# Optimization experiments

Measured on AMD Instinct MI355X. Metric: run time of the kernel, lower is better.

The kernel has to match this reference:

```python
import jax, jax.numpy as jnp
import numpy as np

B, N_Q, N_K, DIM = 4, 4096, 4096, 256
INNER = 64
N_TOPK = 3
MINUS_INF = -1e9


def setup_inputs() -> dict:
    key = jax.random.key(0)
    ks = jax.random.split(key, 5)
    q = jax.random.normal(ks[0], (B, N_Q, DIM), dtype=jnp.float32)
    k = jax.random.normal(ks[1], (B, N_K, DIM), dtype=jnp.float32)
    v = jax.random.normal(ks[2], (B, N_K, DIM), dtype=jnp.float32)
    Wq = jax.random.normal(ks[3], (DIM, INNER), dtype=jnp.float32) * 0.02
    Wk = jax.random.normal(ks[4], (DIM, INNER), dtype=jnp.float32) * 0.02
    return {"q": q, "k": k, "v": v, "Wq": Wq, "Wk": Wk}


def reference(q, k, v, Wq, Wk):
    # v is accepted but unused, matching the torch module.
    scale = INNER ** (-0.5)  # dim_head == inner_dim == 64
    qh = (q @ Wq) * scale            # [B, N_Q, 64]
    kh = k @ Wk                      # [B, N_K, 64]
    # heads = 1 -> scores [B, 1, N_Q, N_K]
    scores = jnp.einsum('bqd,bkd->bqk', qh, kh)[:, None]
    # torch.kthvalue(k=N_K - 3) == 4th-largest value per row
    thresh = jax.lax.top_k(scores, N_TOPK + 1)[0][..., N_TOPK:N_TOPK + 1]
    masked = jnp.where(scores < thresh, MINUS_INF, scores)
    return jax.nn.softmax(masked, axis=-1)
```

## Files before the change

### kernel.cpp

```cpp
#include <hip/hip_runtime.h>
#include <hip/hip_bf16.h>
#include <math.h>

typedef float v4f __attribute__((ext_vector_type(4)));
typedef short bf16x8 __attribute__((ext_vector_type(8)));
typedef float f32x16 __attribute__((ext_vector_type(16)));

#define BATCH 4
#define NQ 4096
#define NK 4096
#define DIM 256
#define INNER 64
#define NEG_INF (-3.0e38f)
#define CAP 64

__global__ __launch_bounds__(256) void proj_kernel(
    const float* __restrict__ q, const float* __restrict__ k,
    const float* __restrict__ Wq, const float* __restrict__ Wk,
    float* __restrict__ qh, float* __restrict__ kh,
    ushort* __restrict__ qhb, ushort* __restrict__ khb,
    float* __restrict__ outz)
{
  __shared__ float xs[32 * 260];
  const int bid = blockIdx.x;
  const bool isq = bid < 512;
  const float* X   = isq ? q : k;
  const float* W   = isq ? Wq : Wk;
  float*   out     = isq ? qh : kh;
  const float scale = isq ? 0.125f : 1.0f;
  const int row0 = (isq ? bid : bid - 512) * 32;
  const int t = threadIdx.x;

  #pragma unroll
  for (int it = 0; it < 8; ++it) {
    int idx = it * 256 + t;
    int r = idx >> 6, dq = idx & 63;
    v4f v = *reinterpret_cast<const v4f*>(X + (size_t)(row0 + r) * DIM + dq * 4);
    *reinterpret_cast<v4f*>(&xs[r * 260 + dq * 4]) = v;
  }
  __syncthreads();

  const int i0 = (t & 15) * 4;
  const int rg = t >> 4;
  float acc[2][4];
  #pragma unroll
  for (int p = 0; p < 2; ++p)
    #pragma unroll
    for (int i = 0; i < 4; ++i) acc[p][i] = 0.f;

  for (int d0 = 0; d0 < DIM; d0 += 4) {
    v4f w0 = *reinterpret_cast<const v4f*>(W + (d0 + 0) * INNER + i0);
    v4f w1 = *reinterpret_cast<const v4f*>(W + (d0 + 1) * INNER + i0);
    v4f w2 = *reinterpret_cast<const v4f*>(W + (d0 + 2) * INNER + i0);
    v4f w3 = *reinterpret_cast<const v4f*>(W + (d0 + 3) * INNER + i0);
    #pragma unroll
    for (int p = 0; p < 2; ++p) {
      v4f x = *reinterpret_cast<const v4f*>(&xs[(rg + 16 * p) * 260 + d0]);
      #pragma unroll
      for (int i = 0; i < 4; ++i) {
        float bs = x[0] * w0[i];
        bs = fmaf(x[1], w1[i], bs);
        bs = fmaf(x[2], w2[i], bs);
        bs = fmaf(x[3], w3[i], bs);
        acc[p][i] += bs;
      }
    }
  }

  const int d  = i0 >> 4;
  const int hi = (i0 >> 3) & 1;
  const int e0 = i0 & 7;
  #pragma unroll
  for (int p = 0; p < 2; ++p) {
    v4f o;
    ushort ob[4];
    #pragma unroll
    for (int i = 0; i < 4; ++i) {
      o[i] = acc[p][i] * scale;
      __hip_bfloat16 h = __float2bfloat16(o[i]);
      ob[i] = *reinterpret_cast<ushort*>(&h);
    }
    int rr = rg + 16 * p;
    size_t row = (size_t)(row0 + rr);
    *reinterpret_cast<v4f*>(out + row * INNER + i0) = o;
    if (isq) {
      *reinterpret_cast<uint2*>(qhb + row * INNER + i0) =
          *reinterpret_cast<uint2*>(ob);
    } else {
      size_t off = (size_t)(bid - 512) * 2048 + d * 512 + hi * 256 + rr * 8 + e0;
      *reinterpret_cast<uint2*>(khb + off) = *reinterpret_cast<uint2*>(ob);
    }
  }

  {
    v4f* zp = reinterpret_cast<v4f*>(outz);
    const v4f z = {0.f, 0.f, 0.f, 0.f};
    size_t idx = (size_t)bid * 256 + t;
    #pragma unroll 4
    for (int it = 0; it < 64; ++it)
      zp[idx + (size_t)it * 262144] = z;
  }
}

__device__ __forceinline__ void insert5(float (&v)[5], int (&ix)[5], float x, int xi) {
  bool g0 = x > v[0], g1 = x > v[1], g2 = x > v[2], g3 = x > v[3];
  v[4]  = g3 ? v[3] : x;                 ix[4] = g3 ? ix[3] : xi;
  v[3]  = g3 ? (g2 ? v[2] : x) : v[3];   ix[3] = g3 ? (g2 ? ix[2] : xi) : ix[3];
  v[2]  = g2 ? (g1 ? v[1] : x) : v[2];   ix[2] = g2 ? (g1 ? ix[1] : xi) : ix[2];
  v[1]  = g1 ? (g0 ? v[0] : x) : v[1];   ix[1] = g1 ? (g0 ? ix[0] : xi) : ix[1];
  v[0]  = g0 ? x : v[0];                 ix[0] = g0 ? xi : ix[0];
}

__device__ __forceinline__ void insert8v(float (&v)[8], float x) {
  bool g0 = x > v[0], g1 = x > v[1], g2 = x > v[2], g3 = x > v[3];
  bool g4 = x > v[4], g5 = x > v[5], g6 = x > v[6];
  v[7] = g6 ? v[6] : x;
  v[6] = g6 ? (g5 ? v[5] : x) : v[6];
  v[5] = g5 ? (g4 ? v[4] : x) : v[5];
  v[4] = g4 ? (g3 ? v[3] : x) : v[4];
  v[3] = g3 ? (g2 ? v[2] : x) : v[3];
  v[2] = g2 ? (g1 ? v[1] : x) : v[2];
  v[1] = g1 ? (g0 ? v[0] : x) : v[1];
  v[0] = g0 ? x : v[0];
}

__global__ __launch_bounds__(512) void filter_kernel(
    const ushort* __restrict__ qhb, const ushort* __restrict__ khb,
    const float* __restrict__ qh, const float* __restrict__ kh,
    float* __restrict__ out)
{
  __shared__ float qhf[32][68];
  __shared__ float sm[32][16];
  __shared__ float tau[32];
  __shared__ int   cnt[32];
  __shared__ int   cand[32][CAP];
  __shared__ float exactv[32][CAP];
  __shared__ float w5[32][5];
  __shared__ int   id5[32][6];

  const int t   = threadIdx.x;
  const int bid = blockIdx.x;
  const int wg  = (bid & 7) * 64 + (bid >> 3);
  const int b   = wg >> 7;
  const int q0  = (wg & 127) * 32;
  const int qg  = t >> 6;
  const int kg  = t & 63;
  const int ln  = kg & 31;
  const int hi  = kg >> 5;

  if (t < 256) {
    int row = t >> 3, c8 = (t & 7) * 8;
    const float* src = qh + ((size_t)b * NQ + q0 + row) * INNER + c8;
    *reinterpret_cast<v4f*>(&qhf[row][c8])     = *reinterpret_cast<const v4f*>(src);
    *reinterpret_cast<v4f*>(&qhf[row][c8 + 4]) = *reinterpret_cast<const v4f*>(src + 4);
  }
  if (t < 32) cnt[t] = 0;

  const ushort* qptr = qhb + ((size_t)b * NQ + q0 + ln) * INNER + hi * 8;
  bf16x8 qf0 = *reinterpret_cast<const bf16x8*>(qptr);
  bf16x8 qf1 = *reinterpret_cast<const bf16x8*>(qptr + 16);
  bf16x8 qf2 = *reinterpret_cast<const bf16x8*>(qptr + 32);
  bf16x8 qf3 = *reinterpret_cast<const bf16x8*>(qptr + 48);

  const ushort* ktile = khb + ((size_t)b * 128 + qg * 16) * 2048;

  float smax = NEG_INF;
  for (int t16 = 0; t16 < 16; ++t16) {
    const ushort* tb = ktile + (size_t)t16 * 2048;
    bf16x8 k0 = *reinterpret_cast<const bf16x8*>(tb +        kg * 8);
    bf16x8 k1 = *reinterpret_cast<const bf16x8*>(tb +  512 + kg * 8);
    bf16x8 k2 = *reinterpret_cast<const bf16x8*>(tb + 1024 + kg * 8);
    bf16x8 k3 = *reinterpret_cast<const bf16x8*>(tb + 1536 + kg * 8);

    f32x16 acc = {0.f, 0.f, 0.f, 0.f, 0.f, 0.f, 0.f, 0.f,
                  0.f, 0.f, 0.f, 0.f, 0.f, 0.f, 0.f, 0.f};
    acc = __builtin_amdgcn_mfma_f32_32x32x16_bf16(k0, qf0, acc, 0, 0, 0);
    acc = __builtin_amdgcn_mfma_f32_32x32x16_bf16(k1, qf1, acc, 0, 0, 0);
    acc = __builtin_amdgcn_mfma_f32_32x32x16_bf16(k2, qf2, acc, 0, 0, 0);
    acc = __builtin_amdgcn_mfma_f32_32x32x16_bf16(k3, qf3, acc, 0, 0, 0);

    float m0 = fmaxf(fmaxf(acc[0],  acc[1]),  fmaxf(acc[2],  acc[3]));
    float m1 = fmaxf(fmaxf(acc[4],  acc[5]),  fmaxf(acc[6],  acc[7]));
    float m2 = fmaxf(fmaxf(acc[8],  acc[9]),  fmaxf(acc[10], acc[11]));
    float m3 = fmaxf(fmaxf(acc[12], acc[13]), fmaxf(acc[14], acc[15]));
    smax = fmaxf(smax, fmaxf(fmaxf(m0, m1), fmaxf(m2, m3)));
  }
  sm[ln][qg * 2 + hi] = smax;
  __syncthreads();

  if (t < 32) {
    float rv[8];
    #pragma unroll
    for (int j = 0; j < 8; ++j) rv[j] = NEG_INF;
    #pragma unroll
    for (int s = 0; s < 16; ++s) {
      float x = sm[t][s];
      if (x > rv[7]) insert8v(rv, x);
    }
    tau[t] = rv[7];
  }
  __syncthreads();

  const float tl = tau[ln];
  for (int t16 = 0; t16 < 16; ++t16) {
    const ushort* tb = ktile + (size_t)t16 * 2048;
    bf16x8 k0 = *reinterpret_cast<const bf16x8*>(tb +        kg * 8);
    bf16x8 k1 = *reinterpret_cast<const bf16x8*>(tb +  512 + kg * 8);
    bf16x8 k2 = *reinterpret_cast<const bf16x8*>(tb + 1024 + kg * 8);
    bf16x8 k3 = *reinterpret_cast<const bf16x8*>(tb + 1536 + kg * 8);

    f32x16 acc = {0.f, 0.f, 0.f, 0.f, 0.f, 0.f, 0.f, 0.f,
                  0.f, 0.f, 0.f, 0.f, 0.f, 0.f, 0.f, 0.f};
    acc = __builtin_amdgcn_mfma_f32_32x32x16_bf16(k0, qf0, acc, 0, 0, 0);
    acc = __builtin_amdgcn_mfma_f32_32x32x16_bf16(k1, qf1, acc, 0, 0, 0);
    acc = __builtin_amdgcn_mfma_f32_32x32x16_bf16(k2, qf2, acc, 0, 0, 0);
    acc = __builtin_amdgcn_mfma_f32_32x32x16_bf16(k3, qf3, acc, 0, 0, 0);

    const int kb0 = qg * 512 + t16 * 32 + 4 * hi;
#define CHK(r) { float x_ = acc[r]; \
                 if (x_ >= tl) { \
                   int p_ = atomicAdd(&cnt[ln], 1); \
                   if (p_ < CAP) cand[ln][p_] = kb0 + ((r) & 3) + 8 * ((r) >> 2); } }
    CHK(0)  CHK(1)  CHK(2)  CHK(3)
    CHK(4)  CHK(5)  CHK(6)  CHK(7)
    CHK(8)  CHK(9)  CHK(10) CHK(11)
    CHK(12) CHK(13) CHK(14) CHK(15)
#undef CHK
  }
  __syncthreads();

  {
    int row = t >> 4, j0 = t & 15;
    int n = min(cnt[row], CAP);
    for (int jj = j0; jj < n; jj += 16) {
      int idx = cand[row][jj];
      const float* kcol = kh + ((size_t)b * NK + idx) * INNER;
      float acc = 0.f;
      #pragma unroll
      for (int dd = 0; dd < INNER; dd += 4) {
        v4f kv = *reinterpret_cast<const v4f*>(kcol + dd);
        v4f qv = *reinterpret_cast<const v4f*>(&qhf[row][dd]);
        float bs = qv[0] * kv[0];
        bs = fmaf(qv[1], kv[1], bs);
        bs = fmaf(qv[2], kv[2], bs);
        bs = fmaf(qv[3], kv[3], bs);
        acc += bs;
      }
      exactv[row][jj] = acc;
    }
  }
  __syncthreads();

  if (t < 32) {
    int n = min(cnt[t], CAP);
    float rv[5]; int ri[5];
    #pragma unroll
    for (int j = 0; j < 5; ++j) { rv[j] = NEG_INF; ri[j] = 0; }
    for (int j = 0; j < n; ++j) {
      float x = exactv[t][j];
      if (x > rv[4]) insert5(rv, ri, x, cand[t][j]);
    }
    bool inc4 = (rv[4] >= rv[3]);
    float e1 = expf(rv[1] - rv[0]);
    float e2 = expf(rv[2] - rv[0]);
    float e3 = expf(rv[3] - rv[0]);
    float e4 = inc4 ? expf(rv[4] - rv[0]) : 0.0f;
    float inv = 1.0f / (1.0f + e1 + e2 + e3 + e4);
    w5[t][0] = inv;      w5[t][1] = e1 * inv;  w5[t][2] = e2 * inv;
    w5[t][3] = e3 * inv; w5[t][4] = e4 * inv;
    #pragma unroll
    for (int j = 0; j < 5; ++j) id5[t][j] = ri[j];
    id5[t][5] = inc4 ? 5 : 4;
  }
  __syncthreads();

  if (t < 160) {
    int row = t / 5, j = t % 5;
    if (j < id5[row][5]) {
      float* obase = out + ((size_t)b * NQ + q0) * (size_t)NK;
      obase[(size_t)row * NK + id5[row][j]] = w5[row][j];
    }
  }
}

extern "C" void kernel_launch(void* const* d_in, const int* in_sizes, int n_in,
                              void* d_out, int out_size, void* d_ws, size_t ws_size,
                              hipStream_t stream) {
  const float* q  = (const float*)d_in[0];
  const float* k  = (const float*)d_in[1];
  const float* Wq = (const float*)d_in[3];
  const float* Wk = (const float*)d_in[4];

  const size_t NE = (size_t)BATCH * NQ * INNER;
  float*  qh  = (float*)d_ws;
  float*  kh  = qh + NE;
  ushort* qhb = (ushort*)(kh + NE);
  ushort* khb = qhb + NE;

  proj_kernel<<<1024, 256, 0, stream>>>(q, k, Wq, Wk, qh, kh, qhb, khb,
                                        (float*)d_out);
  filter_kernel<<<512, 512, 0, stream>>>(qhb, khb, qh, kh, (float*)d_out);
}
```

Baseline: 143.1 us.

## Process 64 query rows per filter block and split zero-fill into separate blocks

The filter kernel now handles 64 query rows per workgroup, two 32-row MFMA tiles sharing each loaded K fragment. This halves K-tile reloads and the grid size. The zero-fill of the output moves from the projection blocks into 2048 dedicated blocks, so the fill runs in parallel with projection instead of after it. The cost is more registers and shared memory per filter block and only 256 filter workgroups, which may underfill the GPU.

```diff
diff --git a/kernel.cpp b/kernel.cpp
--- a/kernel.cpp
+++ b/kernel.cpp
@@ -14,7 +14,7 @@
 #define NEG_INF (-3.0e38f)
 #define CAP 64
 
-__global__ __launch_bounds__(256) void proj_kernel(
+__global__ __launch_bounds__(256) void projfill_kernel(
     const float* __restrict__ q, const float* __restrict__ k,
     const float* __restrict__ Wq, const float* __restrict__ Wk,
     float* __restrict__ qh, float* __restrict__ kh,
@@ -23,13 +23,24 @@
 {
   __shared__ float xs[32 * 260];
   const int bid = blockIdx.x;
+  const int t = threadIdx.x;
+
+  if (bid >= 1024) {
+    v4f* zp = reinterpret_cast<v4f*>(outz);
+    const v4f z = {0.f, 0.f, 0.f, 0.f};
+    size_t idx = (size_t)(bid - 1024) * 256 + t;
+    #pragma unroll 8
+    for (int it = 0; it < 32; ++it)
+      zp[idx + (size_t)it * 524288] = z;
+    return;
+  }
+
   const bool isq = bid < 512;
   const float* X   = isq ? q : k;
   const float* W   = isq ? Wq : Wk;
   float*   out     = isq ? qh : kh;
   const float scale = isq ? 0.125f : 1.0f;
   const int row0 = (isq ? bid : bid - 512) * 32;
-  const int t = threadIdx.x;
 
   #pragma unroll
   for (int it = 0; it < 8; ++it) {
@@ -90,15 +101,6 @@
       size_t off = (size_t)(bid - 512) * 2048 + d * 512 + hi * 256 + rr * 8 + e0;
       *reinterpret_cast<uint2*>(khb + off) = *reinterpret_cast<uint2*>(ob);
     }
-  }
-
-  {
-    v4f* zp = reinterpret_cast<v4f*>(outz);
-    const v4f z = {0.f, 0.f, 0.f, 0.f};
-    size_t idx = (size_t)bid * 256 + t;
-    #pragma unroll 4
-    for (int it = 0; it < 64; ++it)
-      zp[idx + (size_t)it * 262144] = z;
   }
 }
 
@@ -129,42 +131,47 @@
     const float* __restrict__ qh, const float* __restrict__ kh,
     float* __restrict__ out)
 {
-  __shared__ float qhf[32][68];
-  __shared__ float sm[32][16];
-  __shared__ float tau[32];
-  __shared__ int   cnt[32];
-  __shared__ int   cand[32][CAP];
-  __shared__ float exactv[32][CAP];
-  __shared__ float w5[32][5];
-  __shared__ int   id5[32][6];
+  __shared__ float qhf[64][68];
+  __shared__ float sm[64][16];
+  __shared__ float tau[64];
+  __shared__ int   cnt[64];
+  __shared__ int   cand[64][CAP];
+  __shared__ float exactv[64][CAP];
+  __shared__ float w5[64][5];
+  __shared__ int   id5[64][6];
 
   const int t   = threadIdx.x;
   const int bid = blockIdx.x;
-  const int wg  = (bid & 7) * 64 + (bid >> 3);
-  const int b   = wg >> 7;
-  const int q0  = (wg & 127) * 32;
+  const int wg  = (bid & 7) * 32 + (bid >> 3);
+  const int b   = wg >> 6;
+  const int q0  = (wg & 63) * 64;
   const int qg  = t >> 6;
   const int kg  = t & 63;
   const int ln  = kg & 31;
   const int hi  = kg >> 5;
 
-  if (t < 256) {
+  {
     int row = t >> 3, c8 = (t & 7) * 8;
     const float* src = qh + ((size_t)b * NQ + q0 + row) * INNER + c8;
     *reinterpret_cast<v4f*>(&qhf[row][c8])     = *reinterpret_cast<const v4f*>(src);
     *reinterpret_cast<v4f*>(&qhf[row][c8 + 4]) = *reinterpret_cast<const v4f*>(src + 4);
   }
-  if (t < 32) cnt[t] = 0;
-
-  const ushort* qptr = qhb + ((size_t)b * NQ + q0 + ln) * INNER + hi * 8;
-  bf16x8 qf0 = *reinterpret_cast<const bf16x8*>(qptr);
-  bf16x8 qf1 = *reinterpret_cast<const bf16x8*>(qptr + 16);
-  bf16x8 qf2 = *reinterpret_cast<const bf16x8*>(qptr + 32);
-  bf16x8 qf3 = *reinterpret_cast<const bf16x8*>(qptr + 48);
+  if (t < 64) cnt[t] = 0;
+
+  const ushort* qptrA = qhb + ((size_t)b * NQ + q0 + ln) * INNER + hi * 8;
+  const ushort* qptrB = qptrA + 32 * INNER;
+  bf16x8 qfA0 = *reinterpret_cast<const bf16x8*>(qptrA);
+  bf16x8 qfA1 = *reinterpret_cast<const bf16x8*>(qptrA + 16);
+  bf16x8 qfA2 = *reinterpret_cast<const bf16x8*>(qptrA + 32);
+  bf16x8 qfA3 = *reinterpret_cast<const bf16x8*>(qptrA + 48);
+  bf16x8 qfB0 = *reinterpret_cast<const bf16x8*>(qptrB);
+  bf16x8 qfB1 = *reinterpret_cast<const bf16x8*>(qptrB + 16);
+  bf16x8 qfB2 = *reinterpret_cast<const bf16x8*>(qptrB + 32);
+  bf16x8 qfB3 = *reinterpret_cast<const bf16x8*>(qptrB + 48);
 
   const ushort* ktile = khb + ((size_t)b * 128 + qg * 16) * 2048;
 
-  float smax = NEG_INF;
+  float smaxA = NEG_INF, smaxB = NEG_INF;
   for (int t16 = 0; t16 < 16; ++t16) {
     const ushort* tb = ktile + (size_t)t16 * 2048;
     bf16x8 k0 = *reinterpret_cast<const bf16x8*>(tb +        kg * 8);
@@ -172,23 +179,33 @@
     bf16x8 k2 = *reinterpret_cast<const bf16x8*>(tb + 1024 + kg * 8);
     bf16x8 k3 = *reinterpret_cast<const bf16x8*>(tb + 1536 + kg * 8);
 
-    f32x16 acc = {0.f, 0.f, 0.f, 0.f, 0.f, 0.f, 0.f, 0.f,
-                  0.f, 0.f, 0.f, 0.f, 0.f, 0.f, 0.f, 0.f};
-    acc = __builtin_amdgcn_mfma_f32_32x32x16_bf16(k0, qf0, acc, 0, 0, 0);
-    acc = __builtin_amdgcn_mfma_f32_32x32x16_bf16(k1, qf1, acc, 0, 0, 0);
-    acc = __builtin_amdgcn_mfma_f32_32x32x16_bf16(k2, qf2, acc, 0, 0, 0);
-    acc = __builtin_amdgcn_mfma_f32_32x32x16_bf16(k3, qf3, acc, 0, 0, 0);
-
-    float m0 = fmaxf(fmaxf(acc[0],  acc[1]),  fmaxf(acc[2],  acc[3]));
-    float m1 = fmaxf(fmaxf(acc[4],  acc[5]),  fmaxf(acc[6],  acc[7]));
-    float m2 = fmaxf(fmaxf(acc[8],  acc[9]),  fmaxf(acc[10], acc[11]));
-    float m3 = fmaxf(fmaxf(acc[12], acc[13]), fmaxf(acc[14], acc[15]));
-    smax = fmaxf(smax, fmaxf(fmaxf(m0, m1), fmaxf(m2, m3)));
-  }
-  sm[ln][qg * 2 + hi] = smax;
-  __syncthreads();
-
-  if (t < 32) {
+    f32x16 aA = {0.f,0.f,0.f,0.f,0.f,0.f,0.f,0.f,0.f,0.f,0.f,0.f,0.f,0.f,0.f,0.f};
+    f32x16 aB = {0.f,0.f,0.f,0.f,0.f,0.f,0.f,0.f,0.f,0.f,0.f,0.f,0.f,0.f,0.f,0.f};
+    aA = __builtin_amdgcn_mfma_f32_32x32x16_bf16(k0, qfA0, aA, 0, 0, 0);
+    aA = __builtin_amdgcn_mfma_f32_32x32x16_bf16(k1, qfA1, aA, 0, 0, 0);
+    aA = __builtin_amdgcn_mfma_f32_32x32x16_bf16(k2, qfA2, aA, 0, 0, 0);
+    aA = __builtin_amdgcn_mfma_f32_32x32x16_bf16(k3, qfA3, aA, 0, 0, 0);
+    aB = __builtin_amdgcn_mfma_f32_32x32x16_bf16(k0, qfB0, aB, 0, 0, 0);
+    aB = __builtin_amdgcn_mfma_f32_32x32x16_bf16(k1, qfB1, aB, 0, 0, 0);
+    aB = __builtin_amdgcn_mfma_f32_32x32x16_bf16(k2, qfB2, aB, 0, 0, 0);
+    aB = __builtin_amdgcn_mfma_f32_32x32x16_bf16(k3, qfB3, aB, 0, 0, 0);
+
+    float a0 = fmaxf(fmaxf(aA[0],  aA[1]),  fmaxf(aA[2],  aA[3]));
+    float a1 = fmaxf(fmaxf(aA[4],  aA[5]),  fmaxf(aA[6],  aA[7]));
+    float a2 = fmaxf(fmaxf(aA[8],  aA[9]),  fmaxf(aA[10], aA[11]));
+    float a3 = fmaxf(fmaxf(aA[12], aA[13]), fmaxf(aA[14], aA[15]));
+    smaxA = fmaxf(smaxA, fmaxf(fmaxf(a0, a1), fmaxf(a2, a3)));
+    float b0 = fmaxf(fmaxf(aB[0],  aB[1]),  fmaxf(aB[2],  aB[3]));
+    float b1 = fmaxf(fmaxf(aB[4],  aB[5]),  fmaxf(aB[6],  aB[7]));
+    float b2 = fmaxf(fmaxf(aB[8],  aB[9]),  fmaxf(aB[10], aB[11]));
+    float b3 = fmaxf(fmaxf(aB[12], aB[13]), fmaxf(aB[14], aB[15]));
+    smaxB = fmaxf(smaxB, fmaxf(fmaxf(b0, b1), fmaxf(b2, b3)));
+  }
+  sm[ln][qg * 2 + hi]      = smaxA;
+  sm[32 + ln][qg * 2 + hi] = smaxB;
+  __syncthreads();
+
+  if (t < 64) {
     float rv[8];
     #pragma unroll
     for (int j = 0; j < 8; ++j) rv[j] = NEG_INF;
@@ -201,7 +218,8 @@
   }
   __syncthreads();
 
-  const float tl = tau[ln];
+  const float tlA = tau[ln];
+  const float tlB = tau[32 + ln];
   for (int t16 = 0; t16 < 16; ++t16) {
     const ushort* tb = ktile + (size_t)t16 * 2048;
     bf16x8 k0 = *reinterpret_cast<const bf16x8*>(tb +        kg * 8);
@@ -209,30 +227,43 @@
     bf16x8 k2 = *reinterpret_cast<const bf16x8*>(tb + 1024 + kg * 8);
     bf16x8 k3 = *reinterpret_cast<const bf16x8*>(tb + 1536 + kg * 8);
 
-    f32x16 acc = {0.f, 0.f, 0.f, 0.f, 0.f, 0.f, 0.f, 0.f,
-                  0.f, 0.f, 0.f, 0.f, 0.f, 0.f, 0.f, 0.f};
-    acc = __builtin_amdgcn_mfma_f32_32x32x16_bf16(k0, qf0, acc, 0, 0, 0);
-    acc = __builtin_amdgcn_mfma_f32_32x32x16_bf16(k1, qf1, acc, 0, 0, 0);
-    acc = __builtin_amdgcn_mfma_f32_32x32x16_bf16(k2, qf2, acc, 0, 0, 0);
-    acc = __builtin_amdgcn_mfma_f32_32x32x16_bf16(k3, qf3, acc, 0, 0, 0);
+    f32x16 aA = {0.f,0.f,0.f,0.f,0.f,0.f,0.f,0.f,0.f,0.f,0.f,0.f,0.f,0.f,0.f,0.f};
+    f32x16 aB = {0.f,0.f,0.f,0.f,0.f,0.f,0.f,0.f,0.f,0.f,0.f,0.f,0.f,0.f,0.f,0.f};
+    aA = __builtin_amdgcn_mfma_f32_32x32x16_bf16(k0, qfA0, aA, 0, 0, 0);
+    aA = __builtin_amdgcn_mfma_f32_32x32x16_bf16(k1, qfA1, aA, 0, 0, 0);
+    aA = __builtin_amdgcn_mfma_f32_32x32x16_bf16(k2, qfA2, aA, 0, 0, 0);
+    aA = __builtin_amdgcn_mfma_f32_32x32x16_bf16(k3, qfA3, aA, 0, 0, 0);
+    aB = __builtin_amdgcn_mfma_f32_32x32x16_bf16(k0, qfB0, aB, 0, 0, 0);
+    aB = __builtin_amdgcn_mfma_f32_32x32x16_bf16(k1, qfB1, aB, 0, 0, 0);
+    aB = __builtin_amdgcn_mfma_f32_32x32x16_bf16(k2, qfB2, aB, 0, 0, 0);
+    aB = __builtin_amdgcn_mfma_f32_32x32x16_bf16(k3, qfB3, aB, 0, 0, 0);
 
     const int kb0 = qg * 512 + t16 * 32 + 4 * hi;
-#define CHK(r) { float x_ = acc[r]; \
-                 if (x_ >= tl) { \
-                   int p_ = atomicAdd(&cnt[ln], 1); \
-                   if (p_ < CAP) cand[ln][p_] = kb0 + ((r) & 3) + 8 * ((r) >> 2); } }
-    CHK(0)  CHK(1)  CHK(2)  CHK(3)
-    CHK(4)  CHK(5)  CHK(6)  CHK(7)
-    CHK(8)  CHK(9)  CHK(10) CHK(11)
-    CHK(12) CHK(13) CHK(14) CHK(15)
-#undef CHK
+#define CHKA(r) { float x_ = aA[r]; \
+                  if (x_ >= tlA) { \
+                    int p_ = atomicAdd(&cnt[ln], 1); \
+                    if (p_ < CAP) cand[ln][p_] = kb0 + ((r) & 3) + 8 * ((r) >> 2); } }
+#define CHKB(r) { float x_ = aB[r]; \
+                  if (x_ >= tlB) { \
+                    int p_ = atomicAdd(&cnt[32 + ln], 1); \
+                    if (p_ < CAP) cand[32 + ln][p_] = kb0 + ((r) & 3) + 8 * ((r) >> 2); } }
+    CHKA(0)  CHKA(1)  CHKA(2)  CHKA(3)
+    CHKA(4)  CHKA(5)  CHKA(6)  CHKA(7)
+    CHKA(8)  CHKA(9)  CHKA(10) CHKA(11)
+    CHKA(12) CHKA(13) CHKA(14) CHKA(15)
+    CHKB(0)  CHKB(1)  CHKB(2)  CHKB(3)
+    CHKB(4)  CHKB(5)  CHKB(6)  CHKB(7)
+    CHKB(8)  CHKB(9)  CHKB(10) CHKB(11)
+    CHKB(12) CHKB(13) CHKB(14) CHKB(15)
+#undef CHKA
+#undef CHKB
   }
   __syncthreads();
 
   {
-    int row = t >> 4, j0 = t & 15;
+    int row = t >> 3, j0 = t & 7;
     int n = min(cnt[row], CAP);
-    for (int jj = j0; jj < n; jj += 16) {
+    for (int jj = j0; jj < n; jj += 8) {
       int idx = cand[row][jj];
       const float* kcol = kh + ((size_t)b * NK + idx) * INNER;
       float acc = 0.f;
@@ -251,7 +282,7 @@
   }
   __syncthreads();
 
-  if (t < 32) {
+  if (t < 64) {
     int n = min(cnt[t], CAP);
     float rv[5]; int ri[5];
     #pragma unroll
@@ -274,7 +305,7 @@
   }
   __syncthreads();
 
-  if (t < 160) {
+  if (t < 320) {
     int row = t / 5, j = t % 5;
     if (j < id5[row][5]) {
       float* obase = out + ((size_t)b * NQ + q0) * (size_t)NK;
@@ -297,7 +328,7 @@
   ushort* qhb = (ushort*)(kh + NE);
   ushort* khb = qhb + NE;
 
-  proj_kernel<<<1024, 256, 0, stream>>>(q, k, Wq, Wk, qh, kh, qhb, khb,
-                                        (float*)d_out);
-  filter_kernel<<<512, 512, 0, stream>>>(qhb, khb, qh, kh, (float*)d_out);
-}
+  projfill_kernel<<<3072, 256, 0, stream>>>(q, k, Wq, Wk, qh, kh, qhb, khb,
+                                            (float*)d_out);
+  filter_kernel<<<256, 512, 0, stream>>>(qhb, khb, qh, kh, (float*)d_out);
+}
```

Result: slower. 152.2 us (+6.4%).
